# Performance work log

Hardware: AMD Instinct MI355X
Metric: run time of the kernel (lower is better)

The kernel has to match this reference:

```python
import jax, jax.numpy as jnp
import numpy as np
from jax import lax

B, T, E, H, O = 256, 128, 256, 256, 1024


def setup_inputs() -> dict:
    key = jax.random.key(0)
    ks = jax.random.split(key, 7)
    s_ih = 1.0 / np.sqrt(H)
    inp = {
        "x": jax.random.normal(ks[0], (B, T, E), dtype=jnp.float32),
        # PyTorch LSTM params (single layer), gate order i, f, g, o
        "w_ih": jax.random.uniform(ks[1], (4 * H, E), minval=-s_ih, maxval=s_ih, dtype=jnp.float32),
        "w_hh": jax.random.uniform(ks[2], (4 * H, H), minval=-s_ih, maxval=s_ih, dtype=jnp.float32),
        "b_ih": jax.random.uniform(ks[3], (4 * H,), minval=-s_ih, maxval=s_ih, dtype=jnp.float32),
        "b_hh": jax.random.uniform(ks[4], (4 * H,), minval=-s_ih, maxval=s_ih, dtype=jnp.float32),
        "w_fc": jax.random.uniform(ks[5], (O, H * T), minval=-1.0 / np.sqrt(H * T), maxval=1.0 / np.sqrt(H * T), dtype=jnp.float32),
        "b_fc": jax.random.uniform(ks[6], (O,), minval=-1.0 / np.sqrt(H * T), maxval=1.0 / np.sqrt(H * T), dtype=jnp.float32),
    }
    return inp


def reference(x, w_ih, w_hh, b_ih, b_hh, w_fc, b_fc):
    Bn, Tn, _ = x.shape
    Hn = w_hh.shape[1]
    # Precompute input-to-gate projections for all timesteps: [B, T, 4H]
    x_gates = jnp.einsum("bte,ge->btg", x, w_ih) + b_ih + b_hh

    def step(carry, xg_t):
        h, c = carry
        gates = xg_t + h @ w_hh.T  # [B, 4H]
        i, f, g, o = jnp.split(gates, 4, axis=-1)
        i = jax.nn.sigmoid(i)
        f = jax.nn.sigmoid(f)
        g = jnp.tanh(g)
        o = jax.nn.sigmoid(o)
        c = f * c + i * g
        h = o * jnp.tanh(c)
        return (h, c), h

    h0 = jnp.zeros((Bn, Hn), dtype=x.dtype)
    c0 = jnp.zeros((Bn, Hn), dtype=x.dtype)
    # scan over time axis
    _, hs = lax.scan(step, (h0, c0), jnp.swapaxes(x_gates, 0, 1))  # hs: [T, B, H]
    lstm_out = jnp.swapaxes(hs, 0, 1).reshape(Bn, -1)  # [B, T*H]
    return lstm_out @ w_fc.T + b_fc  # [B, O]
```

## Files before the change

kernel.cpp:

```cpp
#include <hip/hip_runtime.h>
#include <math.h>

#define Bsz 256
#define Tsz 128
#define Esz 256
#define Hsz 256
#define Gsz 1024
#define Osz 1024
#define KFC 32768
#define KSPLIT 32
#define NBI 16
#define NHJ 16

__device__ __forceinline__ float sigmoidf_(float x) { return 1.0f / (1.0f + expf(-x)); }

__global__ void transpose_kn(const float* __restrict__ in, float* __restrict__ out, int N, int K) {
    int i = blockIdx.x * blockDim.x + threadIdx.x;
    if (i >= N * K) return;
    int k = i / N;
    int n = i - k * N;
    out[i] = in[n * K + k];
}

template <int BIAS>
__global__ __launch_bounds__(256, 2) void gemm128(const float* __restrict__ A, int lda,
                                                  const float* __restrict__ W, int ldw,
                                                  const float* __restrict__ bih,
                                                  const float* __restrict__ bhh,
                                                  float* __restrict__ C, int ldc,
                                                  int klen) {
    __shared__ float As[16][132];
    __shared__ float Bs[16][132];
    int tid = threadIdx.x;
    int tm = tid & 15, tn = tid >> 4;
    int lrow = tid >> 1, lkc = (tid & 1) * 8;
    int kbase = blockIdx.z * klen;
    const float* Ap = A + (size_t)(blockIdx.x * 128 + lrow) * lda + kbase + lkc;
    const float* Wp = W + (size_t)(blockIdx.y * 128 + lrow) * ldw + kbase + lkc;
    float4 pa0, pa1, pb0, pb1;
    pa0 = *(const float4*)(Ap);     pa1 = *(const float4*)(Ap + 4);
    pb0 = *(const float4*)(Wp);     pb1 = *(const float4*)(Wp + 4);
    float acc[8][8] = {};
    int nc = klen >> 4;
    for (int c = 0; c < nc; ++c) {
        __syncthreads();
        As[lkc + 0][lrow] = pa0.x; As[lkc + 1][lrow] = pa0.y; As[lkc + 2][lrow] = pa0.z; As[lkc + 3][lrow] = pa0.w;
        As[lkc + 4][lrow] = pa1.x; As[lkc + 5][lrow] = pa1.y; As[lkc + 6][lrow] = pa1.z; As[lkc + 7][lrow] = pa1.w;
        Bs[lkc + 0][lrow] = pb0.x; Bs[lkc + 1][lrow] = pb0.y; Bs[lkc + 2][lrow] = pb0.z; Bs[lkc + 3][lrow] = pb0.w;
        Bs[lkc + 4][lrow] = pb1.x; Bs[lkc + 5][lrow] = pb1.y; Bs[lkc + 6][lrow] = pb1.z; Bs[lkc + 7][lrow] = pb1.w;
        __syncthreads();
        if (c + 1 < nc) {
            int off = (c + 1) * 16;
            pa0 = *(const float4*)(Ap + off);     pa1 = *(const float4*)(Ap + off + 4);
            pb0 = *(const float4*)(Wp + off);     pb1 = *(const float4*)(Wp + off + 4);
        }
#pragma unroll
        for (int kk = 0; kk < 16; ++kk) {
            float4 a0 = *(const float4*)&As[kk][tm * 8];
            float4 a1 = *(const float4*)&As[kk][tm * 8 + 4];
            float4 b0 = *(const float4*)&Bs[kk][tn * 8];
            float4 b1 = *(const float4*)&Bs[kk][tn * 8 + 4];
            float ar[8] = {a0.x, a0.y, a0.z, a0.w, a1.x, a1.y, a1.z, a1.w};
            float br[8] = {b0.x, b0.y, b0.z, b0.w, b1.x, b1.y, b1.z, b1.w};
#pragma unroll
            for (int i = 0; i < 8; ++i)
#pragma unroll
                for (int j = 0; j < 8; ++j) acc[i][j] += ar[i] * br[j];
        }
    }
    int row0 = blockIdx.x * 128 + tm * 8;
    int col0 = blockIdx.y * 128 + tn * 8;
    float* Cout = C + (BIAS ? 0 : (size_t)blockIdx.z * Bsz * Osz);
    float bias[8];
#pragma unroll
    for (int j = 0; j < 8; ++j) bias[j] = BIAS ? (bih[col0 + j] + bhh[col0 + j]) : 0.f;
#pragma unroll
    for (int i = 0; i < 8; ++i) {
        float4 o0, o1;
        o0.x = acc[i][0] + bias[0]; o0.y = acc[i][1] + bias[1];
        o0.z = acc[i][2] + bias[2]; o0.w = acc[i][3] + bias[3];
        o1.x = acc[i][4] + bias[4]; o1.y = acc[i][5] + bias[5];
        o1.z = acc[i][6] + bias[6]; o1.w = acc[i][7] + bias[7];
        *(float4*)&Cout[(size_t)(row0 + i) * ldc + col0] = o0;
        *(float4*)&Cout[(size_t)(row0 + i) * ldc + col0 + 4] = o1;
    }
}

__global__ void reduce_out(const float* __restrict__ P, const float* __restrict__ bfc,
                           float* __restrict__ out) {
    int i = blockIdx.x * blockDim.x + threadIdx.x;
    if (i >= Bsz * Osz) return;
    float s = bfc[i & (Osz - 1)];
#pragma unroll
    for (int ks = 0; ks < KSPLIT; ++ks) s += P[(size_t)ks * Bsz * Osz + i];
    out[i] = s;
}

__global__ __launch_bounds__(1024) void lstm_scan_coop2(
    const float* __restrict__ xg,
    const float* __restrict__ whhT,
    float* __restrict__ hs,
    float* hbuf,
    unsigned int* cnt)
{
    const int hj = blockIdx.x, bi = blockIdx.y;
    const int tid = threadIdx.x;
    __shared__ float HT[256][16];
    __shared__ float Pp[16][16][68];
    __shared__ float gbuf[4][16][16];

    const int ks   = tid >> 6;
    const int rgrp = (tid >> 4) & 3;
    const int cgrp = tid & 15;
    const int colbase = (cgrp >> 2) * 256 + hj * 16 + (cgrp & 3) * 4;
    float4 w[16];
#pragma unroll
    for (int kk = 0; kk < 16; ++kk)
        w[kk] = *(const float4*)&whhT[(size_t)(ks * 16 + kk) * Gsz + colbase];

    const int gq = tid >> 8, rq = (tid >> 4) & 15, hq = tid & 15;
    const int r_a = tid >> 4, hc_a = tid & 15;
    float c_state = 0.f;
    float* hb = hbuf + (size_t)bi * 8192;
    unsigned int* myc = cnt + bi * 32;

    for (int t = 0; t < Tsz; ++t) {
        const int p = t & 1;
        {
            const unsigned int* src = (const unsigned int*)(hb + (size_t)p * 4096);
            float* HTf = &HT[0][0];
#pragma unroll
            for (int i = 0; i < 4; ++i) {
                unsigned int u = __hip_atomic_load(src + tid + 1024 * i,
                                                   __ATOMIC_RELAXED, __HIP_MEMORY_SCOPE_AGENT);
                HTf[tid + 1024 * i] = __uint_as_float(u);
            }
        }
        float xgv = xg[((size_t)(bi * 16 + rq) * Tsz + t) * Gsz + gq * 256 + hj * 16 + hq];
        __syncthreads();
        float acc[4][4] = {};
#pragma unroll
        for (int kk = 0; kk < 16; ++kk) {
            float4 hv = *(const float4*)&HT[ks * 16 + kk][rgrp * 4];
            float hr[4] = {hv.x, hv.y, hv.z, hv.w};
            float wr[4] = {w[kk].x, w[kk].y, w[kk].z, w[kk].w};
#pragma unroll
            for (int i = 0; i < 4; ++i)
#pragma unroll
                for (int j = 0; j < 4; ++j) acc[i][j] += hr[i] * wr[j];
        }
#pragma unroll
        for (int i = 0; i < 4; ++i)
            *(float4*)&Pp[ks][rgrp * 4 + i][cgrp * 4] =
                make_float4(acc[i][0], acc[i][1], acc[i][2], acc[i][3]);
        __syncthreads();
        {
            float s = 0.f;
#pragma unroll
            for (int sl = 0; sl < 16; ++sl) s += Pp[sl][rq][gq * 16 + hq];
            s += xgv;
            s = (gq == 2) ? tanhf(s) : sigmoidf_(s);
            gbuf[gq][rq][hq] = s;
        }
        __syncthreads();
        if (tid < 256) {
            float gi = gbuf[0][r_a][hc_a];
            float gf = gbuf[1][r_a][hc_a];
            float gg = gbuf[2][r_a][hc_a];
            float go = gbuf[3][r_a][hc_a];
            c_state = gf * c_state + gi * gg;
            float hval = go * tanhf(c_state);
            hs[(size_t)(bi * 16 + r_a) * KFC + t * Hsz + hj * 16 + hc_a] = hval;
            __hip_atomic_store((unsigned int*)hb + (size_t)(p ^ 1) * 4096 + (hj * 16 + hc_a) * 16 + r_a,
                               __float_as_uint(hval),
                               __ATOMIC_RELAXED, __HIP_MEMORY_SCOPE_AGENT);
        }
        __syncthreads();
        if (t < Tsz - 1) {
            if (tid == 0) {
                __hip_atomic_fetch_add(myc, 1u, __ATOMIC_RELAXED, __HIP_MEMORY_SCOPE_AGENT);
                unsigned target = 16u * (unsigned)(t + 1);
                long guard = 0;
                while (__hip_atomic_load(myc, __ATOMIC_RELAXED, __HIP_MEMORY_SCOPE_AGENT) < target) {
                    if (++guard > (1L << 22)) break;
                }
            }
            __syncthreads();
        }
    }
}

__device__ __forceinline__ void matvec_acc(const float* __restrict__ WT, const float4* HV, int len,
                                           int col0, int col1, float a0[4], float a1[4]) {
    float wa0[4], wa1[4], wb0[4], wb1[4];
#pragma unroll
    for (int q = 0; q < 4; ++q) { wa0[q] = WT[q * Gsz + col0]; wa1[q] = WT[q * Gsz + col1]; }
    for (int k = 0; k < len; k += 8) {
#pragma unroll
        for (int q = 0; q < 4; ++q) {
            int kk = (k + 4 + q) & (len - 1);
            wb0[q] = WT[kk * Gsz + col0]; wb1[q] = WT[kk * Gsz + col1];
        }
#pragma unroll
        for (int q = 0; q < 4; ++q) {
            float4 hq = HV[k + q];
            a0[0] += wa0[q] * hq.x; a0[1] += wa0[q] * hq.y; a0[2] += wa0[q] * hq.z; a0[3] += wa0[q] * hq.w;
            a1[0] += wa1[q] * hq.x; a1[1] += wa1[q] * hq.y; a1[2] += wa1[q] * hq.z; a1[3] += wa1[q] * hq.w;
        }
#pragma unroll
        for (int q = 0; q < 4; ++q) {
            int kk = (k + 8 + q) & (len - 1);
            wa0[q] = WT[kk * Gsz + col0]; wa1[q] = WT[kk * Gsz + col1];
        }
#pragma unroll
        for (int q = 0; q < 4; ++q) {
            float4 hq = HV[k + 4 + q];
            a0[0] += wb0[q] * hq.x; a0[1] += wb0[q] * hq.y; a0[2] += wb0[q] * hq.z; a0[3] += wb0[q] * hq.w;
            a1[0] += wb1[q] * hq.x; a1[1] += wb1[q] * hq.y; a1[2] += wb1[q] * hq.z; a1[3] += wb1[q] * hq.w;
        }
    }
}

template <int XGF>
__global__ __launch_bounds__(512) void lstm_scan(const float* __restrict__ xgin,
                                                 const float* __restrict__ whhT,
                                                 const float* __restrict__ wihT,
                                                 const float* __restrict__ bih,
                                                 const float* __restrict__ bhh,
                                                 float* __restrict__ hs) {
    int j = threadIdx.x;
    int b0 = blockIdx.x * 4;
    int col0 = j, col1 = j + 512;
    __shared__ float4 h4[Hsz];
    __shared__ float4 x4[Esz];
    __shared__ float fo[2][4][Hsz];
    float c[4] = {0.f, 0.f, 0.f, 0.f};
    float bias0 = 0.f, bias1 = 0.f;
    if (XGF) { bias0 = bih[col0] + bhh[col0]; bias1 = bih[col1] + bhh[col1]; }
    if (j < Hsz) h4[j] = make_float4(0.f, 0.f, 0.f, 0.f);
    __syncthreads();
    for (int t = 0; t < Tsz; ++t) {
        float a0[4], a1[4];
        if (XGF) {
#pragma unroll
            for (int r = 0; r < 4; ++r) { a0[r] = bias0; a1[r] = bias1; }
            if (j < Esz) {
                float4 v;
                v.x = xgin[((size_t)(b0 + 0) * Tsz + t) * Esz + j];
                v.y = xgin[((size_t)(b0 + 1) * Tsz + t) * Esz + j];
                v.z = xgin[((size_t)(b0 + 2) * Tsz + t) * Esz + j];
                v.w = xgin[((size_t)(b0 + 3) * Tsz + t) * Esz + j];
                x4[j] = v;
            }
            __syncthreads();
            matvec_acc(wihT, x4, Esz, col0, col1, a0, a1);
        } else {
#pragma unroll
            for (int r = 0; r < 4; ++r) {
                a0[r] = xgin[((size_t)(b0 + r) * Tsz + t) * Gsz + col0];
                a1[r] = xgin[((size_t)(b0 + r) * Tsz + t) * Gsz + col1];
            }
        }
        matvec_acc(whhT, h4, Hsz, col0, col1, a0, a1);
        if (j < Hsz) {
#pragma unroll
            for (int r = 0; r < 4; ++r) { a0[r] = sigmoidf_(a0[r]); a1[r] = tanhf(a1[r]); }
        } else {
#pragma unroll
            for (int r = 0; r < 4; ++r) {
                fo[0][r][j - Hsz] = sigmoidf_(a0[r]);
                fo[1][r][j - Hsz] = sigmoidf_(a1[r]);
            }
        }
        __syncthreads();
        if (j < Hsz) {
            float hv[4];
#pragma unroll
            for (int r = 0; r < 4; ++r) {
                float f = fo[0][r][j], o = fo[1][r][j];
                c[r] = f * c[r] + a0[r] * a1[r];
                hv[r] = o * tanhf(c[r]);
                hs[(size_t)(b0 + r) * KFC + t * Hsz + j] = hv[r];
            }
            h4[j] = make_float4(hv[0], hv[1], hv[2], hv[3]);
        }
        __syncthreads();
    }
}

extern "C" void kernel_launch(void* const* d_in, const int* in_sizes, int n_in,
                              void* d_out, int out_size, void* d_ws, size_t ws_size,
                              hipStream_t stream) {
    const float* x    = (const float*)d_in[0];
    const float* w_ih = (const float*)d_in[1];
    const float* w_hh = (const float*)d_in[2];
    const float* b_ih = (const float*)d_in[3];
    const float* b_hh = (const float*)d_in[4];
    const float* w_fc = (const float*)d_in[5];
    const float* b_fc = (const float*)d_in[6];
    float* out = (float*)d_out;
    char* ws = (char*)d_ws;

    const size_t XG_BYTES = (size_t)Bsz * Tsz * Gsz * 4;
    const size_t WT_BYTES = (size_t)Esz * Gsz * 4;
    const size_t HS_BYTES = (size_t)Bsz * KFC * 4;
    const size_t P_BYTES  = (size_t)KSPLIT * Bsz * Osz * 4;
    const size_t HB_BYTES = (size_t)NBI * 2 * 4096 * 4;
    const size_t CNT_BYTES = (size_t)NBI * 32 * 4;
    bool fast = ws_size >= XG_BYTES + WT_BYTES + HS_BYTES + P_BYTES + HB_BYTES + CNT_BYTES;

    const int KLEN = KFC / KSPLIT;

    if (fast) {
        float* xg   = (float*)(ws);
        float* whhT = (float*)(ws + XG_BYTES);
        float* hsb  = (float*)(ws + XG_BYTES + WT_BYTES);
        float* part = (float*)(ws + XG_BYTES + WT_BYTES + HS_BYTES);
        float* hbuf = (float*)(ws + XG_BYTES + WT_BYTES + HS_BYTES + P_BYTES);
        unsigned int* cnt = (unsigned int*)(ws + XG_BYTES + WT_BYTES + HS_BYTES + P_BYTES + HB_BYTES);
        hipMemsetAsync(hbuf, 0, HB_BYTES + CNT_BYTES, stream);
        transpose_kn<<<(Esz * Gsz + 255) / 256, 256, 0, stream>>>(w_hh, whhT, Gsz, Esz);
        gemm128<1><<<dim3(Bsz * Tsz / 128, Gsz / 128, 1), 256, 0, stream>>>(
            x, Esz, w_ih, Esz, b_ih, b_hh, xg, Gsz, Esz);
        lstm_scan_coop2<<<dim3(NHJ, NBI), 1024, 0, stream>>>(xg, whhT, hsb, hbuf, cnt);
        gemm128<0><<<dim3(Bsz / 128, Osz / 128, KSPLIT), 256, 0, stream>>>(
            hsb, KFC, w_fc, KFC, nullptr, nullptr, part, Osz, KLEN);
        reduce_out<<<(Bsz * Osz + 255) / 256, 256, 0, stream>>>(part, b_fc, out);
    } else {
        float* whhT = (float*)(ws);
        float* wihT = (float*)(ws + WT_BYTES);
        float* hsb  = (float*)(ws + 2 * WT_BYTES);
        float* part = (float*)(ws + 2 * WT_BYTES + HS_BYTES);
        transpose_kn<<<(Esz * Gsz + 255) / 256, 256, 0, stream>>>(w_hh, whhT, Gsz, Esz);
        transpose_kn<<<(Esz * Gsz + 255) / 256, 256, 0, stream>>>(w_ih, wihT, Gsz, Esz);
        lstm_scan<1><<<Bsz / 4, 512, 0, stream>>>(x, whhT, wihT, b_ih, b_hh, hsb);
        gemm128<0><<<dim3(Bsz / 128, Osz / 128, KSPLIT), 256, 0, stream>>>(
            hsb, KFC, w_fc, KFC, nullptr, nullptr, part, Osz, KLEN);
        reduce_out<<<(Bsz * Osz + 255) / 256, 256, 0, stream>>>(part, b_fc, out);
    }
}
```

Measured before the change: 1.132 ms.

## Replace counter barrier with per-block step flags in cooperative LSTM scan

Replaces the shared atomic counter barrier, where every block did a fetch_add and thread 0 spun, with per-block step flags. Each block publishes its step and 16 threads poll the 16 sibling flags in parallel before loading h. This removes contention on a single counter and moves the wait to the start of the next step. It also widens the h-buffer loads to 64-bit atomics and changes the partial-sum smem padding to 76. The flags are relaxed stores issued without a release fence after the h stores, which risks reading stale h values.

Result: slower. 1.319 ms (+16.6%).

```diff
diff --git a/kernel.cpp b/kernel.cpp
--- a/kernel.cpp
+++ b/kernel.cpp
@@ -11,6 +11,7 @@
 #define KSPLIT 32
 #define NBI 16
 #define NHJ 16
+#define PPAD 76
 
 __device__ __forceinline__ float sigmoidf_(float x) { return 1.0f / (1.0f + expf(-x)); }
 
@@ -96,17 +97,17 @@
     out[i] = s;
 }
 
-__global__ __launch_bounds__(1024) void lstm_scan_coop2(
+__global__ __launch_bounds__(1024) void lstm_scan_coop3(
     const float* __restrict__ xg,
     const float* __restrict__ whhT,
     float* __restrict__ hs,
     float* hbuf,
-    unsigned int* cnt)
+    unsigned int* flags)
 {
     const int hj = blockIdx.x, bi = blockIdx.y;
     const int tid = threadIdx.x;
     __shared__ float HT[256][16];
-    __shared__ float Pp[16][16][68];
+    __shared__ float Pp[16][16][PPAD];
     __shared__ float gbuf[4][16][16];
 
     const int ks   = tid >> 6;
@@ -122,19 +123,25 @@
     const int r_a = tid >> 4, hc_a = tid & 15;
     float c_state = 0.f;
     float* hb = hbuf + (size_t)bi * 8192;
-    unsigned int* myc = cnt + bi * 32;
+    unsigned int* fl = flags + (size_t)bi * NHJ * 16;
 
     for (int t = 0; t < Tsz; ++t) {
         const int p = t & 1;
+        if (t > 0 && tid < NHJ) {
+            unsigned target = (unsigned)t;
+            long guard = 0;
+            while (__hip_atomic_load(fl + tid * 16, __ATOMIC_RELAXED, __HIP_MEMORY_SCOPE_AGENT) < target) {
+                if (++guard > (1L << 22)) break;
+            }
+        }
+        __syncthreads();
         {
-            const unsigned int* src = (const unsigned int*)(hb + (size_t)p * 4096);
-            float* HTf = &HT[0][0];
-#pragma unroll
-            for (int i = 0; i < 4; ++i) {
-                unsigned int u = __hip_atomic_load(src + tid + 1024 * i,
-                                                   __ATOMIC_RELAXED, __HIP_MEMORY_SCOPE_AGENT);
-                HTf[tid + 1024 * i] = __uint_as_float(u);
-            }
+            const unsigned long long* src = (const unsigned long long*)(hb + (size_t)p * 4096);
+            unsigned long long* dst = (unsigned long long*)&HT[0][0];
+            unsigned long long v0 = __hip_atomic_load(src + tid,        __ATOMIC_RELAXED, __HIP_MEMORY_SCOPE_AGENT);
+            unsigned long long v1 = __hip_atomic_load(src + tid + 1024, __ATOMIC_RELAXED, __HIP_MEMORY_SCOPE_AGENT);
+            dst[tid] = v0;
+            dst[tid + 1024] = v1;
         }
         float xgv = xg[((size_t)(bi * 16 + rq) * Tsz + t) * Gsz + gq * 256 + hj * 16 + hq];
         __syncthreads();
@@ -176,16 +183,9 @@
                                __ATOMIC_RELAXED, __HIP_MEMORY_SCOPE_AGENT);
         }
         __syncthreads();
-        if (t < Tsz - 1) {
-            if (tid == 0) {
-                __hip_atomic_fetch_add(myc, 1u, __ATOMIC_RELAXED, __HIP_MEMORY_SCOPE_AGENT);
-                unsigned target = 16u * (unsigned)(t + 1);
-                long guard = 0;
-                while (__hip_atomic_load(myc, __ATOMIC_RELAXED, __HIP_MEMORY_SCOPE_AGENT) < target) {
-                    if (++guard > (1L << 22)) break;
-                }
-            }
-            __syncthreads();
+        if (tid == 0 && t < Tsz - 1) {
+            __hip_atomic_store(fl + hj * 16, (unsigned)(t + 1),
+                               __ATOMIC_RELAXED, __HIP_MEMORY_SCOPE_AGENT);
         }
     }
 }
@@ -306,8 +306,8 @@
     const size_t HS_BYTES = (size_t)Bsz * KFC * 4;
     const size_t P_BYTES  = (size_t)KSPLIT * Bsz * Osz * 4;
     const size_t HB_BYTES = (size_t)NBI * 2 * 4096 * 4;
-    const size_t CNT_BYTES = (size_t)NBI * 32 * 4;
-    bool fast = ws_size >= XG_BYTES + WT_BYTES + HS_BYTES + P_BYTES + HB_BYTES + CNT_BYTES;
+    const size_t FL_BYTES = (size_t)NBI * NHJ * 16 * 4;
+    bool fast = ws_size >= XG_BYTES + WT_BYTES + HS_BYTES + P_BYTES + HB_BYTES + FL_BYTES;
 
     const int KLEN = KFC / KSPLIT;
 
@@ -317,12 +317,12 @@
         float* hsb  = (float*)(ws + XG_BYTES + WT_BYTES);
         float* part = (float*)(ws + XG_BYTES + WT_BYTES + HS_BYTES);
         float* hbuf = (float*)(ws + XG_BYTES + WT_BYTES + HS_BYTES + P_BYTES);
-        unsigned int* cnt = (unsigned int*)(ws + XG_BYTES + WT_BYTES + HS_BYTES + P_BYTES + HB_BYTES);
-        hipMemsetAsync(hbuf, 0, HB_BYTES + CNT_BYTES, stream);
+        unsigned int* flags = (unsigned int*)(ws + XG_BYTES + WT_BYTES + HS_BYTES + P_BYTES + HB_BYTES);
+        hipMemsetAsync(hbuf, 0, HB_BYTES + FL_BYTES, stream);
         transpose_kn<<<(Esz * Gsz + 255) / 256, 256, 0, stream>>>(w_hh, whhT, Gsz, Esz);
         gemm128<1><<<dim3(Bsz * Tsz / 128, Gsz / 128, 1), 256, 0, stream>>>(
             x, Esz, w_ih, Esz, b_ih, b_hh, xg, Gsz, Esz);
-        lstm_scan_coop2<<<dim3(NHJ, NBI), 1024, 0, stream>>>(xg, whhT, hsb, hbuf, cnt);
+        lstm_scan_coop3<<<dim3(NHJ, NBI), 1024, 0, stream>>>(xg, whhT, hsb, hbuf, flags);
         gemm128<0><<<dim3(Bsz / 128, Osz / 128, KSPLIT), 256, 0, stream>>>(
             hsb, KFC, w_fc, KFC, nullptr, nullptr, part, Osz, KLEN);
         reduce_out<<<(Bsz * Osz + 255) / 256, 256, 0, stream>>>(part, b_fc, out);
```
